# Performance work log

Measured on AMD Instinct MI355X. Metric: run time of the kernel, lower is better.

## Reference

```python
import jax, jax.numpy as jnp
import numpy as np

B, D, L = 16384, 2048, 6

def setup_inputs() -> dict:
    key = jax.random.key(0)
    kx, kw = jax.random.split(key)
    x = jax.random.normal(kx, (B, D), dtype=jnp.float32)
    # cross weights: xavier_normal on (D,1) -> std = sqrt(2/(D+1)); stacked [L, D]
    std = float(np.sqrt(2.0 / (D + 1)))
    W = jax.random.normal(kw, (L, D), dtype=jnp.float32) * std
    b = jnp.zeros((L, D), dtype=jnp.float32)  # bias params init to zeros
    return {"x": x, "W": W, "b": b}

def reference(x, W, b):
    # Original per layer: x_l = (x0 @ x_l^T) @ w_i + b_i + x_l
    # Algebraically identical: x_l = x0 * (x_l . w_i) + b_i + x_l  (scalar per row)
    x_l = x
    for i in range(W.shape[0]):
        s = jnp.einsum('bd,d->b', x_l, W[i])          # [B]
        x_l = x * s[:, None] + b[i][None, :] + x_l     # [B, D]
    return x_l
```

## Files before the change

kernel.cpp:

```cpp
#include <hip/hip_runtime.h>

#define B_ROWS   16384
#define D_DIM    2048
#define L_LAYERS 6

#define THREADS  512
#define WPB      (THREADS / 64)
#define ROWS_PER_WAVE 4
#define TOTAL_WAVES (B_ROWS / ROWS_PER_WAVE)
#define BLOCKS   (TOTAL_WAVES / WPB)
#define PRE_THREADS 1024
#define WS_FLOATS   (D_DIM + L_LAYERS)

typedef float f32x4 __attribute__((ext_vector_type(4)));


__global__ __launch_bounds__(PRE_THREADS) void precompute_Ue(
    const float* __restrict__ W,
    const float* __restrict__ b,
    float* __restrict__ ws)
{
    __shared__ float red[PRE_THREADS / 64][L_LAYERS];
    const int t    = threadIdx.x;
    const int lane = t & 63;
    const int wid  = t >> 6;
    const int base = t * 2;

    float2 prefix = make_float2(0.f, 0.f);
    float e_red[L_LAYERS];
    #pragma unroll
    for (int l = 0; l < L_LAYERS; ++l) {
        const float2 wv = *(const float2*)(W + l * D_DIM + base);
        const float2 bv = *(const float2*)(b + l * D_DIM + base);
        e_red[l] = prefix.x * wv.x + prefix.y * wv.y;
        prefix.x += bv.x; prefix.y += bv.y;
    }
    *(float2*)(ws + base) = prefix;
    #pragma unroll
    for (int l = 0; l < L_LAYERS; ++l) {
        float v = e_red[l];
        #pragma unroll
        for (int off = 32; off >= 1; off >>= 1) v += __shfl_xor(v, off, 64);
        if (lane == 0) red[wid][l] = v;
    }
    __syncthreads();
    if (t < L_LAYERS) {
        float s = 0.f;
        #pragma unroll
        for (int w = 0; w < PRE_THREADS / 64; ++w) s += red[w][t];
        ws[D_DIM + t] = s;
    }
}

template <bool USE_WS>
__global__ __launch_bounds__(THREADS, 2) void cross_rows(
    const float* __restrict__ x,
    const float* __restrict__ W,
    const float* __restrict__ b,
    const float* __restrict__ ws,
    float* __restrict__ out)
{
    __shared__ float Wl[L_LAYERS][D_DIM];
    __shared__ float Ul[D_DIM];
    __shared__ float eLs[L_LAYERS];
    __shared__ float red[WPB][L_LAYERS];

    const int t    = threadIdx.x;
    const int lane = t & 63;
    const int wid  = t >> 6;
    const int gw   = blockIdx.x * WPB + wid;
    const float* xr = x + (size_t)gw * ROWS_PER_WAVE * D_DIM;
    float* orow     = out + (size_t)gw * ROWS_PER_WAVE * D_DIM;
    const int eoff  = lane * 4;

    float4 A[8], B[8];

    #pragma unroll
    for (int j = 0; j < 8; ++j) A[j] = *(const float4*)(xr + j * 256 + eoff);
    #pragma unroll
    for (int j = 0; j < 8; ++j) B[j] = *(const float4*)(xr + D_DIM + j * 256 + eoff);

    {
        const int base = t * 4;
        #pragma unroll
        for (int l = 0; l < L_LAYERS; ++l)
            *(float4*)&Wl[l][base] = *(const float4*)(W + l * D_DIM + base);
    }
    if constexpr (USE_WS) {
        const int base = t * 4;
        *(float4*)&Ul[base] = *(const float4*)(ws + base);
        if (t < L_LAYERS) eLs[t] = ws[D_DIM + t];
    } else {
        const int base = t * 4;
        float4 prefix = make_float4(0.f, 0.f, 0.f, 0.f);
        float e_red[L_LAYERS];
        #pragma unroll
        for (int l = 0; l < L_LAYERS; ++l) {
            const float4 wv = *(const float4*)(W + l * D_DIM + base);
            const float4 bv = *(const float4*)(b + l * D_DIM + base);
            e_red[l] = prefix.x * wv.x + prefix.y * wv.y
                     + prefix.z * wv.z + prefix.w * wv.w;
            prefix.x += bv.x; prefix.y += bv.y;
            prefix.z += bv.z; prefix.w += bv.w;
        }
        *(float4*)&Ul[base] = prefix;
        #pragma unroll
        for (int l = 0; l < L_LAYERS; ++l) {
            float v = e_red[l];
            #pragma unroll
            for (int off = 32; off >= 1; off >>= 1) v += __shfl_xor(v, off, 64);
            if (lane == 0) red[wid][l] = v;
        }
        __syncthreads();
        if (t < L_LAYERS) {
            float s = 0.f;
            #pragma unroll
            for (int w = 0; w < WPB; ++w) s += red[w][t];
            eLs[t] = s;
        }
    }
    __syncthreads();

    auto loadRow = [&](float4 (&xv)[8], const float* p) {
        #pragma unroll
        for (int j = 0; j < 8; ++j) xv[j] = *(const float4*)(p + j * 256 + eoff);
    };

    auto dotsC = [&](const float4 (&xv)[8]) -> float {
        float p[L_LAYERS];
        #pragma unroll
        for (int l = 0; l < L_LAYERS; ++l) {
            float a = 0.f;
            #pragma unroll
            for (int j = 0; j < 8; ++j) {
                const float4 wv = *(const float4*)&Wl[l][j * 256 + eoff];
                a += xv[j].x * wv.x + xv[j].y * wv.y
                   + xv[j].z * wv.z + xv[j].w * wv.w;
            }
            p[l] = a;
        }
        #pragma unroll
        for (int off = 32; off >= 1; off >>= 1) {
            #pragma unroll
            for (int l = 0; l < L_LAYERS; ++l)
                p[l] += __shfl_xor(p[l], off, 64);
        }
        float c = 1.f;
        #pragma unroll
        for (int l = 0; l < L_LAYERS; ++l)
            c = c * (1.f + p[l]) + eLs[l];
        return c;
    };

    auto applyStore = [&](const float4 (&xv)[8], float c, float* op) {
        #pragma unroll
        for (int j = 0; j < 8; ++j) {
            const float4 uv = *(const float4*)&Ul[j * 256 + eoff];
            f32x4 o;
            o.x = c * xv[j].x + uv.x; o.y = c * xv[j].y + uv.y;
            o.z = c * xv[j].z + uv.z; o.w = c * xv[j].w + uv.w;
            __builtin_nontemporal_store(o, (f32x4*)(op + j * 256 + eoff));
        }
    };

    {
        const float c0 = dotsC(A);
        applyStore(A, c0, orow);
    }
    {
        const float c1 = dotsC(B);
        applyStore(B, c1, orow + D_DIM);
        __builtin_amdgcn_sched_barrier(0);
        loadRow(A, xr + 2 * (size_t)D_DIM);
    }
    {
        const float c2 = dotsC(A);
        applyStore(A, c2, orow + 2 * (size_t)D_DIM);
        __builtin_amdgcn_sched_barrier(0);
        loadRow(B, xr + 3 * (size_t)D_DIM);
    }
    {
        const float c3 = dotsC(B);
        applyStore(B, c3, orow + 3 * (size_t)D_DIM);
    }
}

extern "C" void kernel_launch(void* const* d_in, const int* in_sizes, int n_in,
                              void* d_out, int out_size, void* d_ws, size_t ws_size,
                              hipStream_t stream) {
    (void)in_sizes; (void)n_in; (void)out_size;
    const float* x = (const float*)d_in[0];
    const float* W = (const float*)d_in[1];
    const float* b = (const float*)d_in[2];
    float* out = (float*)d_out;

    const bool use_ws = (d_ws != nullptr) && (ws_size >= WS_FLOATS * sizeof(float));
    if (use_ws) {
        float* ws = (float*)d_ws;
        precompute_Ue<<<dim3(1), dim3(PRE_THREADS), 0, stream>>>(W, b, ws);
        cross_rows<true><<<dim3(BLOCKS), dim3(THREADS), 0, stream>>>(
            x, W, b, ws, out);
    } else {
        cross_rows<false><<<dim3(BLOCKS), dim3(THREADS), 0, stream>>>(
            x, W, b, nullptr, out);
    }
}
```

Baseline: 264.5 us.

## Stream four rows per wave with shared W loads, re-read x for output

Restructures the per-wave loop so all four rows are processed together. Each W float4 read from LDS is reused across the four rows, and the 24 dot-product reductions are batched into one shuffle tree. The x rows are no longer held in registers across the two phases; they are read from global memory a second time when writing the output. This cuts register pressure and drops the occupancy hint from launch bounds, at the cost of a second read of x, which may hit in cache or may double DRAM read traffic.

Result: faster. 251.7 us (-4.9%).

```diff
diff --git a/kernel.cpp b/kernel.cpp
--- a/kernel.cpp
+++ b/kernel.cpp
@@ -53,7 +53,7 @@
 }
 
 template <bool USE_WS>
-__global__ __launch_bounds__(THREADS, 2) void cross_rows(
+__global__ __launch_bounds__(THREADS) void cross_rows(
     const float* __restrict__ x,
     const float* __restrict__ W,
     const float* __restrict__ b,
@@ -68,42 +68,27 @@
     const int t    = threadIdx.x;
     const int lane = t & 63;
     const int wid  = t >> 6;
-    const int gw   = blockIdx.x * WPB + wid;
-    const float* xr = x + (size_t)gw * ROWS_PER_WAVE * D_DIM;
-    float* orow     = out + (size_t)gw * ROWS_PER_WAVE * D_DIM;
-    const int eoff  = lane * 4;
-
-    float4 A[8], B[8];
+    const int sbase = t * 4;
 
     #pragma unroll
-    for (int j = 0; j < 8; ++j) A[j] = *(const float4*)(xr + j * 256 + eoff);
-    #pragma unroll
-    for (int j = 0; j < 8; ++j) B[j] = *(const float4*)(xr + D_DIM + j * 256 + eoff);
-
-    {
-        const int base = t * 4;
-        #pragma unroll
-        for (int l = 0; l < L_LAYERS; ++l)
-            *(float4*)&Wl[l][base] = *(const float4*)(W + l * D_DIM + base);
-    }
+    for (int l = 0; l < L_LAYERS; ++l)
+        *(float4*)&Wl[l][sbase] = *(const float4*)(W + l * D_DIM + sbase);
     if constexpr (USE_WS) {
-        const int base = t * 4;
-        *(float4*)&Ul[base] = *(const float4*)(ws + base);
+        *(float4*)&Ul[sbase] = *(const float4*)(ws + sbase);
         if (t < L_LAYERS) eLs[t] = ws[D_DIM + t];
     } else {
-        const int base = t * 4;
         float4 prefix = make_float4(0.f, 0.f, 0.f, 0.f);
         float e_red[L_LAYERS];
         #pragma unroll
         for (int l = 0; l < L_LAYERS; ++l) {
-            const float4 wv = *(const float4*)(W + l * D_DIM + base);
-            const float4 bv = *(const float4*)(b + l * D_DIM + base);
+            const float4 wv = *(const float4*)(W + l * D_DIM + sbase);
+            const float4 bv = *(const float4*)(b + l * D_DIM + sbase);
             e_red[l] = prefix.x * wv.x + prefix.y * wv.y
                      + prefix.z * wv.z + prefix.w * wv.w;
             prefix.x += bv.x; prefix.y += bv.y;
             prefix.z += bv.z; prefix.w += bv.w;
         }
-        *(float4*)&Ul[base] = prefix;
+        *(float4*)&Ul[sbase] = prefix;
         #pragma unroll
         for (int l = 0; l < L_LAYERS; ++l) {
             float v = e_red[l];
@@ -121,67 +106,64 @@
     }
     __syncthreads();
 
-    auto loadRow = [&](float4 (&xv)[8], const float* p) {
+    const int gw = blockIdx.x * WPB + wid;
+    const float* xr = x + (size_t)gw * ROWS_PER_WAVE * D_DIM;
+    float* orow     = out + (size_t)gw * ROWS_PER_WAVE * D_DIM;
+    const int eoff  = lane * 4;
+
+    float p[ROWS_PER_WAVE][L_LAYERS];
+    #pragma unroll
+    for (int r = 0; r < ROWS_PER_WAVE; ++r)
         #pragma unroll
-        for (int j = 0; j < 8; ++j) xv[j] = *(const float4*)(p + j * 256 + eoff);
-    };
+        for (int l = 0; l < L_LAYERS; ++l) p[r][l] = 0.f;
 
-    auto dotsC = [&](const float4 (&xv)[8]) -> float {
-        float p[L_LAYERS];
+    #pragma unroll 2
+    for (int j = 0; j < 8; ++j) {
+        float4 wv[L_LAYERS];
         #pragma unroll
-        for (int l = 0; l < L_LAYERS; ++l) {
-            float a = 0.f;
-            #pragma unroll
-            for (int j = 0; j < 8; ++j) {
-                const float4 wv = *(const float4*)&Wl[l][j * 256 + eoff];
-                a += xv[j].x * wv.x + xv[j].y * wv.y
-                   + xv[j].z * wv.z + xv[j].w * wv.w;
-            }
-            p[l] = a;
-        }
+        for (int l = 0; l < L_LAYERS; ++l)
+            wv[l] = *(const float4*)&Wl[l][j * 256 + eoff];
         #pragma unroll
-        for (int off = 32; off >= 1; off >>= 1) {
+        for (int r = 0; r < ROWS_PER_WAVE; ++r) {
+            const float4 xv = *(const float4*)(xr + (size_t)r * D_DIM + j * 256 + eoff);
             #pragma unroll
             for (int l = 0; l < L_LAYERS; ++l)
-                p[l] += __shfl_xor(p[l], off, 64);
+                p[r][l] += xv.x * wv[l].x + xv.y * wv[l].y
+                         + xv.z * wv[l].z + xv.w * wv[l].w;
         }
-        float c = 1.f;
+    }
+
+    #pragma unroll
+    for (int off = 32; off >= 1; off >>= 1) {
+        #pragma unroll
+        for (int r = 0; r < ROWS_PER_WAVE; ++r)
+            #pragma unroll
+            for (int l = 0; l < L_LAYERS; ++l)
+                p[r][l] += __shfl_xor(p[r][l], off, 64);
+    }
+
+    float c[ROWS_PER_WAVE];
+    #pragma unroll
+    for (int r = 0; r < ROWS_PER_WAVE; ++r) {
+        float cr = 1.f;
         #pragma unroll
         for (int l = 0; l < L_LAYERS; ++l)
-            c = c * (1.f + p[l]) + eLs[l];
-        return c;
-    };
+            cr = cr * (1.f + p[r][l]) + eLs[l];
+        c[r] = cr;
+    }
 
-    auto applyStore = [&](const float4 (&xv)[8], float c, float* op) {
+    #pragma unroll 2
+    for (int j = 0; j < 8; ++j) {
+        const float4 uv = *(const float4*)&Ul[j * 256 + eoff];
         #pragma unroll
-        for (int j = 0; j < 8; ++j) {
-            const float4 uv = *(const float4*)&Ul[j * 256 + eoff];
+        for (int r = 0; r < ROWS_PER_WAVE; ++r) {
+            const size_t off = (size_t)r * D_DIM + j * 256 + eoff;
+            const float4 xv = *(const float4*)(xr + off);
             f32x4 o;
-            o.x = c * xv[j].x + uv.x; o.y = c * xv[j].y + uv.y;
-            o.z = c * xv[j].z + uv.z; o.w = c * xv[j].w + uv.w;
-            __builtin_nontemporal_store(o, (f32x4*)(op + j * 256 + eoff));
+            o.x = c[r] * xv.x + uv.x; o.y = c[r] * xv.y + uv.y;
+            o.z = c[r] * xv.z + uv.z; o.w = c[r] * xv.w + uv.w;
+            __builtin_nontemporal_store(o, (f32x4*)(orow + off));
         }
-    };
-
-    {
-        const float c0 = dotsC(A);
-        applyStore(A, c0, orow);
-    }
-    {
-        const float c1 = dotsC(B);
-        applyStore(B, c1, orow + D_DIM);
-        __builtin_amdgcn_sched_barrier(0);
-        loadRow(A, xr + 2 * (size_t)D_DIM);
-    }
-    {
-        const float c2 = dotsC(A);
-        applyStore(A, c2, orow + 2 * (size_t)D_DIM);
-        __builtin_amdgcn_sched_barrier(0);
-        loadRow(B, xr + 3 * (size_t)D_DIM);
-    }
-    {
-        const float c3 = dotsC(B);
-        applyStore(B, c3, orow + 3 * (size_t)D_DIM);
     }
 }
 
```
